# Performance work log

Measured on AMD Instinct MI355X. Metric: run time of the kernel, lower is better.

## Reference

```python
import jax, jax.numpy as jnp
import numpy as np

N, C = 16384, 1000


def setup_inputs() -> dict:
    key = jax.random.key(0)
    ks = jax.random.split(key, 10)
    inp = {}
    for i in range(8):
        inp[f"outputs{i+1}"] = jax.random.normal(ks[i], (N, C), dtype=jnp.float32)
    inp["mimic"] = jax.random.normal(ks[8], (N, C), dtype=jnp.float32)
    inp["targets"] = jax.random.randint(ks[9], (N,), 0, C, dtype=jnp.int64)
    inp["n_test"] = N
    return inp


def _margin(x, targets):
    # top-2 margin, zeroed when target is not the argmax value
    top2, _ = jax.lax.top_k(x, 2)                      # [N, 2]
    tgt = jnp.take_along_axis(x, targets[:, None], axis=1)[:, 0]  # [N]
    return jnp.where(tgt == top2[:, 0], top2[:, 0] - top2[:, 1],
                     jnp.zeros((), x.dtype))


def reference(outputs1, outputs2, outputs3, outputs4, outputs5, outputs6,
              outputs7, outputs8, mimic, targets, n_test):
    T = 2.0
    outs = [outputs1, outputs2, outputs3, outputs4,
            outputs5, outputs6, outputs7, outputs8, mimic]
    margins = jnp.stack([_margin(o, targets) for o in outs], axis=1)  # [N, 9]
    out_threshold = jax.nn.softmax(margins / T, axis=1)               # [N, 9]
    max_preds = jnp.max(jnp.stack(outs[:8], axis=0))                  # scalar
    return (max_preds, out_threshold)
```

## Files before the change

kernel.cpp:

```cpp
#include <hip/hip_runtime.h>
#include <math.h>

#define BLOCK 256
#define WPB   (BLOCK / 64)

__global__ __launch_bounds__(BLOCK) void margin_kernel(
    const float* __restrict__ o0, const float* __restrict__ o1,
    const float* __restrict__ o2, const float* __restrict__ o3,
    const float* __restrict__ o4, const float* __restrict__ o5,
    const float* __restrict__ o6, const float* __restrict__ o7,
    const float* __restrict__ o8,
    const int* __restrict__ targets,
    float* __restrict__ out, float* __restrict__ block_max,
    int N, int C)
{
    __shared__ float s_gm[WPB];

    const int lane   = threadIdx.x & 63;
    const int wib    = threadIdx.x >> 6;
    const int row    = blockIdx.x * WPB + wib;
    const int nf4    = C >> 2;

    float gm = -INFINITY;

    if (row < N) {
        const int c = targets[row];
        const unsigned rowoff = (unsigned)row * (unsigned)C;

        float tv[9];
        tv[0] = o0[rowoff + c]; tv[1] = o1[rowoff + c]; tv[2] = o2[rowoff + c];
        tv[3] = o3[rowoff + c]; tv[4] = o4[rowoff + c]; tv[5] = o5[rowoff + c];
        tv[6] = o6[rowoff + c]; tv[7] = o7[rowoff + c]; tv[8] = o8[rowoff + c];

        float m1[9], m2[9];
        #pragma unroll
        for (int k = 0; k < 9; ++k) { m1[k] = -INFINITY; m2[k] = -INFINITY; }

        const float4* p[9] = {
            (const float4*)(o0 + rowoff), (const float4*)(o1 + rowoff),
            (const float4*)(o2 + rowoff), (const float4*)(o3 + rowoff),
            (const float4*)(o4 + rowoff), (const float4*)(o5 + rowoff),
            (const float4*)(o6 + rowoff), (const float4*)(o7 + rowoff),
            (const float4*)(o8 + rowoff) };

        for (int f4 = lane; f4 < nf4; f4 += 64) {
            float4 v[9];
            #pragma unroll
            for (int k = 0; k < 9; ++k) v[k] = p[k][f4];
            #pragma unroll
            for (int k = 0; k < 9; ++k) {
                m2[k] = fmaxf(m2[k], fminf(m1[k], v[k].x)); m1[k] = fmaxf(m1[k], v[k].x);
                m2[k] = fmaxf(m2[k], fminf(m1[k], v[k].y)); m1[k] = fmaxf(m1[k], v[k].y);
                m2[k] = fmaxf(m2[k], fminf(m1[k], v[k].z)); m1[k] = fmaxf(m1[k], v[k].z);
                m2[k] = fmaxf(m2[k], fminf(m1[k], v[k].w)); m1[k] = fmaxf(m1[k], v[k].w);
            }
        }
        if (C & 3) {
            for (int idx = (nf4 << 2) + lane; idx < C; idx += 64) {
                const float* b[9] = {o0,o1,o2,o3,o4,o5,o6,o7,o8};
                #pragma unroll
                for (int k = 0; k < 9; ++k) {
                    float v = b[k][rowoff + idx];
                    m2[k] = fmaxf(m2[k], fminf(m1[k], v)); m1[k] = fmaxf(m1[k], v);
                }
            }
        }

        #pragma unroll
        for (int off = 32; off > 0; off >>= 1) {
            #pragma unroll
            for (int k = 0; k < 9; ++k) {
                float a1 = __shfl_xor(m1[k], off);
                float a2 = __shfl_xor(m2[k], off);
                m2[k] = fmaxf(fmaxf(m2[k], a2), fminf(m1[k], a1));
                m1[k] = fmaxf(m1[k], a1);
            }
        }

        float margin[9];
        #pragma unroll
        for (int k = 0; k < 9; ++k)
            margin[k] = (tv[k] == m1[k]) ? (m1[k] - m2[k]) : 0.0f;

        #pragma unroll
        for (int k = 0; k < 8; ++k) gm = fmaxf(gm, m1[k]);

        float mm = margin[0];
        #pragma unroll
        for (int k = 1; k < 9; ++k) mm = fmaxf(mm, margin[k]);
        float sum = 0.0f;
        #pragma unroll
        for (int k = 0; k < 9; ++k) sum += expf((margin[k] - mm) * 0.5f);
        float inv = 1.0f / sum;

        float msel = margin[0];
        #pragma unroll
        for (int k = 1; k < 9; ++k) msel = (lane == k) ? margin[k] : msel;
        if (lane < 9)
            out[1 + (size_t)row * 9 + lane] = expf((msel - mm) * 0.5f) * inv;
    }

    if (lane == 0) s_gm[wib] = gm;
    __syncthreads();
    if (threadIdx.x == 0) {
        float bg = s_gm[0];
        #pragma unroll
        for (int w = 1; w < WPB; ++w) bg = fmaxf(bg, s_gm[w]);
        block_max[blockIdx.x] = bg;
    }
}

__global__ __launch_bounds__(256) void finalize_kernel(
    const float* __restrict__ block_max, float* __restrict__ out, int n)
{
    __shared__ float s[4];
    const int lane = threadIdx.x & 63;
    float v = -INFINITY;
    for (int i = threadIdx.x; i < n; i += 256) v = fmaxf(v, block_max[i]);
    #pragma unroll
    for (int off = 32; off > 0; off >>= 1) v = fmaxf(v, __shfl_xor(v, off));
    if (lane == 0) s[threadIdx.x >> 6] = v;
    __syncthreads();
    if (threadIdx.x == 0)
        out[0] = fmaxf(fmaxf(s[0], s[1]), fmaxf(s[2], s[3]));
}

extern "C" void kernel_launch(void* const* d_in, const int* in_sizes, int n_in,
                              void* d_out, int out_size, void* d_ws, size_t ws_size,
                              hipStream_t stream) {
    const float* o0 = (const float*)d_in[0];
    const float* o1 = (const float*)d_in[1];
    const float* o2 = (const float*)d_in[2];
    const float* o3 = (const float*)d_in[3];
    const float* o4 = (const float*)d_in[4];
    const float* o5 = (const float*)d_in[5];
    const float* o6 = (const float*)d_in[6];
    const float* o7 = (const float*)d_in[7];
    const float* o8 = (const float*)d_in[8];
    const int* targets = (const int*)d_in[9];
    const int N = in_sizes[9];
    const int C = in_sizes[0] / N;
    float* out = (float*)d_out;
    float* block_max = (float*)d_ws;

    const int grid = (N + WPB - 1) / WPB;
    margin_kernel<<<dim3(grid), dim3(BLOCK), 0, stream>>>(
        o0, o1, o2, o3, o4, o5, o6, o7, o8, targets, out, block_max, N, C);
    finalize_kernel<<<1, 256, 0, stream>>>(block_max, out, grid);
}
```

Before: 503.3 us.

## Assign one block per row and reduce top-2 across waves in shared memory

Each row was handled by one 64-lane wave, with four rows per block. Now a full 256-thread block splits each row, so every thread issues roughly one set of nine float4 loads instead of looping about four times. Per-wave top-2 results are merged through shared memory, and wave 0 computes the softmax and the row max with small shuffle reductions. This targets the serial load latency of the per-wave loop, but adds a block barrier per row, quadruples the block count, and makes finalize reduce N values instead of N/4.

After: 498.8 us. About the same (-0.9%).

```diff
diff --git a/kernel.cpp b/kernel.cpp
--- a/kernel.cpp
+++ b/kernel.cpp
@@ -14,99 +14,105 @@
     float* __restrict__ out, float* __restrict__ block_max,
     int N, int C)
 {
-    __shared__ float s_gm[WPB];
+    __shared__ float s_m1[WPB][12];
+    __shared__ float s_m2[WPB][12];
 
-    const int lane   = threadIdx.x & 63;
-    const int wib    = threadIdx.x >> 6;
-    const int row    = blockIdx.x * WPB + wib;
-    const int nf4    = C >> 2;
+    const int tid  = threadIdx.x;
+    const int lane = tid & 63;
+    const int wib  = tid >> 6;
+    const int row  = blockIdx.x;
+    const int nf4  = C >> 2;
+    const unsigned rowoff = (unsigned)row * (unsigned)C;
 
-    float gm = -INFINITY;
+    float tvv = 0.0f;
+    if (wib == 0 && lane < 9) {
+        const int c = targets[row];
+        const float* tp = o0;
+        tp = (lane == 1) ? o1 : tp;  tp = (lane == 2) ? o2 : tp;
+        tp = (lane == 3) ? o3 : tp;  tp = (lane == 4) ? o4 : tp;
+        tp = (lane == 5) ? o5 : tp;  tp = (lane == 6) ? o6 : tp;
+        tp = (lane == 7) ? o7 : tp;  tp = (lane == 8) ? o8 : tp;
+        tvv = tp[rowoff + c];
+    }
 
-    if (row < N) {
-        const int c = targets[row];
-        const unsigned rowoff = (unsigned)row * (unsigned)C;
+    float m1[9], m2[9];
+    #pragma unroll
+    for (int k = 0; k < 9; ++k) { m1[k] = -INFINITY; m2[k] = -INFINITY; }
 
-        float tv[9];
-        tv[0] = o0[rowoff + c]; tv[1] = o1[rowoff + c]; tv[2] = o2[rowoff + c];
-        tv[3] = o3[rowoff + c]; tv[4] = o4[rowoff + c]; tv[5] = o5[rowoff + c];
-        tv[6] = o6[rowoff + c]; tv[7] = o7[rowoff + c]; tv[8] = o8[rowoff + c];
+    const float4* p[9] = {
+        (const float4*)(o0 + rowoff), (const float4*)(o1 + rowoff),
+        (const float4*)(o2 + rowoff), (const float4*)(o3 + rowoff),
+        (const float4*)(o4 + rowoff), (const float4*)(o5 + rowoff),
+        (const float4*)(o6 + rowoff), (const float4*)(o7 + rowoff),
+        (const float4*)(o8 + rowoff) };
 
-        float m1[9], m2[9];
+    for (int f4 = tid; f4 < nf4; f4 += BLOCK) {
+        float4 v[9];
         #pragma unroll
-        for (int k = 0; k < 9; ++k) { m1[k] = -INFINITY; m2[k] = -INFINITY; }
-
-        const float4* p[9] = {
-            (const float4*)(o0 + rowoff), (const float4*)(o1 + rowoff),
-            (const float4*)(o2 + rowoff), (const float4*)(o3 + rowoff),
-            (const float4*)(o4 + rowoff), (const float4*)(o5 + rowoff),
-            (const float4*)(o6 + rowoff), (const float4*)(o7 + rowoff),
-            (const float4*)(o8 + rowoff) };
-
-        for (int f4 = lane; f4 < nf4; f4 += 64) {
-            float4 v[9];
-            #pragma unroll
-            for (int k = 0; k < 9; ++k) v[k] = p[k][f4];
+        for (int k = 0; k < 9; ++k) v[k] = p[k][f4];
+        #pragma unroll
+        for (int k = 0; k < 9; ++k) {
+            m2[k] = fmaxf(m2[k], fminf(m1[k], v[k].x)); m1[k] = fmaxf(m1[k], v[k].x);
+            m2[k] = fmaxf(m2[k], fminf(m1[k], v[k].y)); m1[k] = fmaxf(m1[k], v[k].y);
+            m2[k] = fmaxf(m2[k], fminf(m1[k], v[k].z)); m1[k] = fmaxf(m1[k], v[k].z);
+            m2[k] = fmaxf(m2[k], fminf(m1[k], v[k].w)); m1[k] = fmaxf(m1[k], v[k].w);
+        }
+    }
+    if (C & 3) {
+        const float* b[9] = {o0,o1,o2,o3,o4,o5,o6,o7,o8};
+        for (int idx = (nf4 << 2) + tid; idx < C; idx += BLOCK) {
             #pragma unroll
             for (int k = 0; k < 9; ++k) {
-                m2[k] = fmaxf(m2[k], fminf(m1[k], v[k].x)); m1[k] = fmaxf(m1[k], v[k].x);
-                m2[k] = fmaxf(m2[k], fminf(m1[k], v[k].y)); m1[k] = fmaxf(m1[k], v[k].y);
-                m2[k] = fmaxf(m2[k], fminf(m1[k], v[k].z)); m1[k] = fmaxf(m1[k], v[k].z);
-                m2[k] = fmaxf(m2[k], fminf(m1[k], v[k].w)); m1[k] = fmaxf(m1[k], v[k].w);
+                float v = b[k][rowoff + idx];
+                m2[k] = fmaxf(m2[k], fminf(m1[k], v)); m1[k] = fmaxf(m1[k], v);
             }
         }
-        if (C & 3) {
-            for (int idx = (nf4 << 2) + lane; idx < C; idx += 64) {
-                const float* b[9] = {o0,o1,o2,o3,o4,o5,o6,o7,o8};
-                #pragma unroll
-                for (int k = 0; k < 9; ++k) {
-                    float v = b[k][rowoff + idx];
-                    m2[k] = fmaxf(m2[k], fminf(m1[k], v)); m1[k] = fmaxf(m1[k], v);
-                }
+    }
+
+    #pragma unroll
+    for (int off = 32; off > 0; off >>= 1) {
+        #pragma unroll
+        for (int k = 0; k < 9; ++k) {
+            float a1 = __shfl_xor(m1[k], off);
+            float a2 = __shfl_xor(m2[k], off);
+            m2[k] = fmaxf(fmaxf(m2[k], a2), fminf(m1[k], a1));
+            m1[k] = fmaxf(m1[k], a1);
+        }
+    }
+
+    if (lane == 0) {
+        #pragma unroll
+        for (int k = 0; k < 9; ++k) { s_m1[wib][k] = m1[k]; s_m2[wib][k] = m2[k]; }
+    }
+    __syncthreads();
+
+    if (wib == 0) {
+        float a1 = -INFINITY, a2 = -INFINITY;
+        if (lane < 9) {
+            a1 = s_m1[0][lane]; a2 = s_m2[0][lane];
+            #pragma unroll
+            for (int w = 1; w < WPB; ++w) {
+                float b1 = s_m1[w][lane], b2 = s_m2[w][lane];
+                a2 = fmaxf(fmaxf(a2, b2), fminf(a1, b1));
+                a1 = fmaxf(a1, b1);
             }
         }
+        float mg = (lane < 9) ? ((tvv == a1) ? (a1 - a2) : 0.0f) : -INFINITY;
 
+        float mm = mg;
         #pragma unroll
-        for (int off = 32; off > 0; off >>= 1) {
-            #pragma unroll
-            for (int k = 0; k < 9; ++k) {
-                float a1 = __shfl_xor(m1[k], off);
-                float a2 = __shfl_xor(m2[k], off);
-                m2[k] = fmaxf(fmaxf(m2[k], a2), fminf(m1[k], a1));
-                m1[k] = fmaxf(m1[k], a1);
-            }
-        }
+        for (int off = 8; off > 0; off >>= 1) mm = fmaxf(mm, __shfl_xor(mm, off));
+        float ex = (lane < 9) ? expf((mg - mm) * 0.5f) : 0.0f;
+        float sum = ex;
+        #pragma unroll
+        for (int off = 8; off > 0; off >>= 1) sum += __shfl_xor(sum, off);
+        if (lane < 9)
+            out[1 + (size_t)row * 9 + lane] = ex / sum;
 
-        float margin[9];
+        float g = (lane < 8) ? a1 : -INFINITY;
         #pragma unroll
-        for (int k = 0; k < 9; ++k)
-            margin[k] = (tv[k] == m1[k]) ? (m1[k] - m2[k]) : 0.0f;
-
-        #pragma unroll
-        for (int k = 0; k < 8; ++k) gm = fmaxf(gm, m1[k]);
-
-        float mm = margin[0];
-        #pragma unroll
-        for (int k = 1; k < 9; ++k) mm = fmaxf(mm, margin[k]);
-        float sum = 0.0f;
-        #pragma unroll
-        for (int k = 0; k < 9; ++k) sum += expf((margin[k] - mm) * 0.5f);
-        float inv = 1.0f / sum;
-
-        float msel = margin[0];
-        #pragma unroll
-        for (int k = 1; k < 9; ++k) msel = (lane == k) ? margin[k] : msel;
-        if (lane < 9)
-            out[1 + (size_t)row * 9 + lane] = expf((msel - mm) * 0.5f) * inv;
-    }
-
-    if (lane == 0) s_gm[wib] = gm;
-    __syncthreads();
-    if (threadIdx.x == 0) {
-        float bg = s_gm[0];
-        #pragma unroll
-        for (int w = 1; w < WPB; ++w) bg = fmaxf(bg, s_gm[w]);
-        block_max[blockIdx.x] = bg;
+        for (int off = 8; off > 0; off >>= 1) g = fmaxf(g, __shfl_xor(g, off));
+        if (lane == 0) block_max[row] = g;
     }
 }
 
@@ -143,8 +149,7 @@
     float* out = (float*)d_out;
     float* block_max = (float*)d_ws;
 
-    const int grid = (N + WPB - 1) / WPB;
-    margin_kernel<<<dim3(grid), dim3(BLOCK), 0, stream>>>(
+    margin_kernel<<<dim3(N), dim3(BLOCK), 0, stream>>>(
         o0, o1, o2, o3, o4, o5, o6, o7, o8, targets, out, block_max, N, C);
-    finalize_kernel<<<1, 256, 0, stream>>>(block_max, out, grid);
+    finalize_kernel<<<1, 256, 0, stream>>>(block_max, out, N);
 }
```
